# Kernel tuning notes

Hardware: AMD Instinct MI355X
Metric: run time of the kernel (lower is better)

Reference implementation:

```python
import jax, jax.numpy as jnp
import numpy as np

OVERLAP_THRESH = 0.5
NEG_POS_RATIO = 3
VARIANCE = (0.1, 0.2)


def point_form(boxes):
    # center-size (cx,cy,w,h) -> corner (xmin,ymin,xmax,ymax)
    return jnp.concatenate([boxes[:, :2] - boxes[:, 2:] / 2,
                            boxes[:, :2] + boxes[:, 2:] / 2], axis=1)


def jaccard(a, b):
    # a: [O,4] corner boxes, b: [P,4] corner boxes -> IoU [O,P]
    lt = jnp.maximum(a[:, None, :2], b[None, :, :2])
    rb = jnp.minimum(a[:, None, 2:], b[None, :, 2:])
    wh = jnp.clip(rb - lt, 0.0)
    inter = wh[..., 0] * wh[..., 1]
    area_a = (a[:, 2] - a[:, 0]) * (a[:, 3] - a[:, 1])
    area_b = (b[:, 2] - b[:, 0]) * (b[:, 3] - b[:, 1])
    return inter / (area_a[:, None] + area_b[None, :] - inter)


def match_one(truths, priors):
    # truths: [O,4] corner form; priors: [P,4] center-size form
    O = truths.shape[0]
    overlaps = jaccard(truths, point_form(priors))          # [O,P]
    best_prior_idx = jnp.argmax(overlaps, axis=1)           # [O]
    best_truth_overlap = jnp.max(overlaps, axis=0)          # [P]
    best_truth_idx = jnp.argmax(overlaps, axis=0)           # [P]
    # force-assign each gt its best prior
    best_truth_overlap = best_truth_overlap.at[best_prior_idx].set(2.0)
    best_truth_idx = best_truth_idx.at[best_prior_idx].set(jnp.arange(O))
    matches = truths[best_truth_idx]                        # [P,4]
    # ARM: labels are all zeros -> conf = 0 + 1 = 1 for matched, 0 otherwise
    conf = jnp.where(best_truth_overlap < OVERLAP_THRESH, 0, 1).astype(jnp.int32)
    # encode(matched, priors, variances)
    g_cxcy = ((matches[:, :2] + matches[:, 2:]) / 2 - priors[:, :2]) / (VARIANCE[0] * priors[:, 2:])
    g_wh = jnp.log((matches[:, 2:] - matches[:, :2]) / priors[:, 2:]) / VARIANCE[1]
    loc = jnp.concatenate([g_cxcy, g_wh], axis=1)           # [P,4]
    return loc, conf


def arm_loss(loc_data, conf_data, priors, targets):
    B, P, _ = loc_data.shape
    truths = targets[:, :, :4]                              # [B,O,4]
    loc_t, conf_t = jax.vmap(lambda t: match_one(t, priors))(truths)
    loc_t = jax.lax.stop_gradient(loc_t)                    # match targets are detached
    conf_t = jax.lax.stop_gradient(conf_t)
    pos = conf_t > 0                                        # [B,P]

    # localization loss: smooth L1 over positive priors, sum reduction
    diff = loc_data - loc_t
    ad = jnp.abs(diff)
    sl1 = jnp.where(ad < 1.0, 0.5 * diff * diff, ad - 0.5)
    loss_l = jnp.sum(sl1 * pos[..., None].astype(loc_data.dtype))

    # per-prior CE for mining and final loss
    lse = jax.nn.logsumexp(conf_data, axis=-1)              # [B,P]
    c_gt = jnp.take_along_axis(conf_data, conf_t[..., None], axis=-1)[..., 0]
    ce = lse - c_gt                                         # [B,P]

    # hard negative mining: rank negatives by CE (positives zeroed out)
    rank_src = jax.lax.stop_gradient(jnp.where(pos, 0.0, ce))
    loss_idx = jnp.argsort(-rank_src, axis=1)
    idx_rank = jnp.argsort(loss_idx, axis=1)
    num_pos = jnp.sum(pos.astype(jnp.int32), axis=1, keepdims=True)  # [B,1]
    num_neg = jnp.minimum(NEG_POS_RATIO * num_pos, P - 1)
    neg = idx_rank < num_neg                                # [B,P]

    mask = (pos | neg).astype(conf_data.dtype)
    loss_c = jnp.sum(ce * mask)

    N = jnp.sum(num_pos).astype(loc_data.dtype)
    return loss_l / N, loss_c / N


def setup_inputs() -> dict:
    key = jax.random.key(0)
    k1, k2, k3, k4, k5, k6 = jax.random.split(key, 6)
    B, P, O = 64, 32768, 16
    loc_data = jax.random.normal(k1, (B, P, 4), dtype=jnp.float32)
    conf_data = jax.random.normal(k2, (B, P, 2), dtype=jnp.float32)
    # priors: center-size form, interior centers, positive w/h
    cxcy = jax.random.uniform(k3, (P, 2), minval=0.05, maxval=0.95)
    wh = jax.random.uniform(k4, (P, 2), minval=0.02, maxval=0.30)
    priors = jnp.concatenate([cxcy, wh], axis=1).astype(jnp.float32)
    # targets: valid corner-form gt boxes with positive area + label column
    c = jax.random.uniform(k5, (B, O, 2), minval=0.1, maxval=0.9)
    s = jax.random.uniform(k6, (B, O, 2), minval=0.05, maxval=0.4)
    mn = jnp.clip(c - s / 2, 0.0, 1.0)
    mx = jnp.clip(c + s / 2, 0.0, 1.0)
    labels = jnp.ones((B, O, 1), dtype=jnp.float32)
    targets = jnp.concatenate([mn, mx, labels], axis=2).astype(jnp.float32)
    return {"loc_data": loc_data, "conf_data": conf_data, "priors": priors, "targets": targets}


def reference(loc_data, conf_data, priors, targets):
    return arm_loss(loc_data, conf_data, priors, targets)
```

## Files before the change

### kernel.cpp

```cpp
#include <hip/hip_runtime.h>
#include <stdint.h>

#define B_ 64
#define P_ 32768
#define O_ 16
#define BP_CHUNK 1024
#define MCHUNK 4
#define MATCH_BLOCKS (P_ / (512 * MCHUNK) * B_)

constexpr float OVERLAP_THRESH = 0.5f;
constexpr int   NEG_POS_RATIO  = 3;
constexpr float VAR0 = 0.1f;
constexpr float VAR1 = 0.2f;

__device__ __forceinline__ unsigned long long umax64(unsigned long long a,
                                                     unsigned long long b) {
    return a > b ? a : b;
}

__global__ __launch_bounds__(256)
void best_prior_kernel(const float* __restrict__ priors,
                       const float* __restrict__ targets,
                       unsigned long long* __restrict__ bp_pack) {
    int b   = blockIdx.y;
    int tid = threadIdx.x;
    int g   = tid >> 4;
    int o   = tid & 15;

    const float* t = targets + ((size_t)b * O_ + o) * 5;
    float tx0 = t[0], ty0 = t[1], tx1 = t[2], ty1 = t[3];
    float ta  = (tx1 - tx0) * (ty1 - ty0);

    int pbase = blockIdx.x * BP_CHUNK + g;
    float bin_ = 0.f, bun_ = 1.f;
    int   bp_  = pbase;

    #pragma unroll 4
    for (int j = 0; j < BP_CHUNK / 16; ++j) {
        int p = pbase + j * 16;
        float4 pr = ((const float4*)priors)[p];
        float px0 = pr.x - pr.z * 0.5f, py0 = pr.y - pr.w * 0.5f;
        float px1 = pr.x + pr.z * 0.5f, py1 = pr.y + pr.w * 0.5f;
        float pa  = (px1 - px0) * (py1 - py0);
        float w = fmaxf(fminf(tx1, px1) - fmaxf(tx0, px0), 0.f);
        float h = fmaxf(fminf(ty1, py1) - fmaxf(ty0, py0), 0.f);
        float in_ = w * h;
        float un_ = ta + pa - in_;
        bool gt = in_ * bun_ > bin_ * un_;
        bin_ = gt ? in_ : bin_;
        bun_ = gt ? un_ : bun_;
        bp_  = gt ? p   : bp_;
    }

    float iou = bin_ / bun_;
    unsigned long long pack =
        ((unsigned long long)__float_as_uint(iou) << 32) | (unsigned)(~bp_);

    pack = umax64(pack, __shfl_xor(pack, 16, 64));
    pack = umax64(pack, __shfl_xor(pack, 32, 64));

    __shared__ unsigned long long sw[4][16];
    int lane = tid & 63, wid = tid >> 6;
    if (lane < 16) sw[wid][lane] = pack;
    __syncthreads();
    if (tid < 16) {
        unsigned long long m = umax64(umax64(sw[0][tid], sw[1][tid]),
                                      umax64(sw[2][tid], sw[3][tid]));
        atomicMax(&bp_pack[(size_t)b * O_ + tid], m);
    }
}

__device__ __forceinline__ float sl1(float d) {
    float ad = fabsf(d);
    return (ad < 1.f) ? 0.5f * d * d : ad - 0.5f;
}

__global__ __launch_bounds__(256)
void match_kernel(const float* __restrict__ loc_data,
                  const float* __restrict__ conf_data,
                  const float* __restrict__ priors,
                  const float* __restrict__ targets,
                  const unsigned* __restrict__ bp_lo,
                  float* __restrict__ rank,
                  int* __restrict__ num_pos,
                  float2* __restrict__ blk_part) {
    int b    = blockIdx.y;
    int tid  = threadIdx.x;

    __shared__ float4 s_box[O_];
    __shared__ float2 s_meta[O_];
    if (tid < O_) {
        const float* t = targets + ((size_t)b * O_ + tid) * 5;
        float x0 = t[0], y0 = t[1], x1 = t[2], y1 = t[3];
        s_box[tid]  = make_float4(x0, y0, x1, y1);
        int bp = (int)~bp_lo[((size_t)b * O_ + tid) * 2];
        s_meta[tid] = make_float2((x1 - x0) * (y1 - y0), __int_as_float(bp));
    }
    __syncthreads();

    float ll = 0.f, ces = 0.f;
    int   pc = 0;

    for (int c = 0; c < MCHUNK; ++c) {
        int pair = blockIdx.x * (256 * MCHUNK) + c * 256 + tid;
        int p0   = pair * 2;

        float4 prA = ((const float4*)priors)[p0];
        float4 prB = ((const float4*)priors)[p0 + 1];
        float4 cd  = ((const float4*)conf_data)[(size_t)b * (P_ / 2) + pair];

        float ax0 = prA.x - prA.z * 0.5f, ay0 = prA.y - prA.w * 0.5f;
        float ax1 = prA.x + prA.z * 0.5f, ay1 = prA.y + prA.w * 0.5f;
        float bx0 = prB.x - prB.z * 0.5f, by0 = prB.y - prB.w * 0.5f;
        float bx1 = prB.x + prB.z * 0.5f, by1 = prB.y + prB.w * 0.5f;
        float aA = (ax1 - ax0) * (ay1 - ay0);
        float aB = (bx1 - bx0) * (by1 - by0);

        float ibA = 0.f, ubA = 1.f, ibB = 0.f, ubB = 1.f;
        int miA = 0, miB = 0, fiA = -1, fiB = -1;

        #pragma unroll
        for (int o = 0; o < O_; ++o) {
            float4 tb4 = s_box[o];
            float2 mt  = s_meta[o];
            float tx0 = tb4.x, ty0 = tb4.y, tx1 = tb4.z, ty1 = tb4.w;
            float ta  = mt.x;
            int   bp  = __float_as_int(mt.y);

            float wA  = fmaxf(fminf(tx1, ax1) - fmaxf(tx0, ax0), 0.f);
            float hA  = fmaxf(fminf(ty1, ay1) - fmaxf(ty0, ay0), 0.f);
            float inA = wA * hA;
            float unA = ta + aA - inA;
            bool  gA  = inA * ubA > ibA * unA;
            ibA = gA ? inA : ibA;  ubA = gA ? unA : ubA;  miA = gA ? o : miA;
            if (bp == p0) fiA = o;

            float wB  = fmaxf(fminf(tx1, bx1) - fmaxf(tx0, bx0), 0.f);
            float hB  = fmaxf(fminf(ty1, by1) - fmaxf(ty0, by0), 0.f);
            float inB = wB * hB;
            float unB = ta + aB - inB;
            bool  gB  = inB * ubB > ibB * unB;
            ibB = gB ? inB : ibB;  ubB = gB ? unB : ubB;  miB = gB ? o : miB;
            if (bp == p0 + 1) fiB = o;
        }

        bool posA = (fiA >= 0) || (2.f * ibA >= ubA);
        bool posB = (fiB >= 0) || (2.f * ibB >= ubB);

        float mA  = fmaxf(cd.x, cd.y);
        float ceA = mA + __logf(1.f + __expf(-fabsf(cd.x - cd.y))) - (posA ? cd.y : cd.x);
        float mB  = fmaxf(cd.z, cd.w);
        float ceB = mB + __logf(1.f + __expf(-fabsf(cd.z - cd.w))) - (posB ? cd.w : cd.z);

        float2 rk;
        rk.x = posA ? 0.f : ceA;
        rk.y = posB ? 0.f : ceB;
        *(float2*)(rank + (size_t)b * P_ + p0) = rk;

        if (posA) {
            int mi = (fiA >= 0) ? fiA : miA;
            float4 tb4 = s_box[mi];
            float pz = ax1 - ax0, pw = ay1 - ay0;
            float cx = (ax0 + ax1) * 0.5f, cy = (ay0 + ay1) * 0.5f;
            float gcx = __fdividef((tb4.x + tb4.z) * 0.5f - cx, VAR0 * pz);
            float gcy = __fdividef((tb4.y + tb4.w) * 0.5f - cy, VAR0 * pw);
            float gw  = __logf(__fdividef(tb4.z - tb4.x, pz)) * (1.f / VAR1);
            float gh  = __logf(__fdividef(tb4.w - tb4.y, pw)) * (1.f / VAR1);
            float4 ld = ((const float4*)loc_data)[(size_t)b * P_ + p0];
            ll  += sl1(ld.x - gcx) + sl1(ld.y - gcy) + sl1(ld.z - gw) + sl1(ld.w - gh);
            ces += ceA;
            pc  += 1;
        }
        if (posB) {
            int mi = (fiB >= 0) ? fiB : miB;
            float4 tb4 = s_box[mi];
            float pz = bx1 - bx0, pw = by1 - by0;
            float cx = (bx0 + bx1) * 0.5f, cy = (by0 + by1) * 0.5f;
            float gcx = __fdividef((tb4.x + tb4.z) * 0.5f - cx, VAR0 * pz);
            float gcy = __fdividef((tb4.y + tb4.w) * 0.5f - cy, VAR0 * pw);
            float gw  = __logf(__fdividef(tb4.z - tb4.x, pz)) * (1.f / VAR1);
            float gh  = __logf(__fdividef(tb4.w - tb4.y, pw)) * (1.f / VAR1);
            float4 ld = ((const float4*)loc_data)[(size_t)b * P_ + p0 + 1];
            ll  += sl1(ld.x - gcx) + sl1(ld.y - gcy) + sl1(ld.z - gw) + sl1(ld.w - gh);
            ces += ceB;
            pc  += 1;
        }
    }

    for (int off = 32; off; off >>= 1) {
        ll  += __shfl_down(ll, off, 64);
        ces += __shfl_down(ces, off, 64);
        pc  += __shfl_down(pc, off, 64);
    }
    __shared__ float sll[4], sce[4];
    __shared__ int   spc[4];
    int wid = tid >> 6;
    if ((tid & 63) == 0) { sll[wid] = ll; sce[wid] = ces; spc[wid] = pc; }
    __syncthreads();
    if (tid == 0) {
        int tp = spc[0] + spc[1] + spc[2] + spc[3];
        float tl = sll[0] + sll[1] + sll[2] + sll[3];
        float tc = sce[0] + sce[1] + sce[2] + sce[3];
        blk_part[blockIdx.y * gridDim.x + blockIdx.x] = make_float2(tl, tc);
        if (tp) atomicAdd(&num_pos[b], tp);
    }
}

__global__ __launch_bounds__(1024)
void topk_kernel(const float* __restrict__ rank,
                 const int* __restrict__ num_pos,
                 const float2* __restrict__ blk_part,
                 unsigned long long* __restrict__ blk_topk,
                 unsigned* __restrict__ counter,
                 float* __restrict__ out) {
    int b   = blockIdx.x;
    int tid = threadIdx.x;
    int np  = num_pos[b];
    int k   = min(NEG_POS_RATIO * np, P_ - 1);

    __shared__ unsigned cnt[2048];
    __shared__ unsigned wsum[16];
    __shared__ unsigned s_pre;
    __shared__ int      s_k;
    __shared__ unsigned s_ticket;
    int lane = tid & 63, wid = tid >> 6;

    double total = 0.0;
    if (k > 0) {
        const uint4* r4 = (const uint4*)(rank + (size_t)b * P_);
        unsigned key[32];
        #pragma unroll
        for (int j = 0; j < 8; ++j) {
            uint4 v = r4[j * 1024 + tid];
            key[j * 4 + 0] = v.x; key[j * 4 + 1] = v.y;
            key[j * 4 + 2] = v.z; key[j * 4 + 3] = v.w;
        }

        unsigned pre = 0;
        int kk = k;
        #pragma unroll
        for (int level = 0; level < 3; ++level) {
            const int shift = (level == 0) ? 21 : (level == 1) ? 10 : 0;
            const int hishf = (level == 1) ? 21 : 10;
            const unsigned fmask = (level == 2) ? 0x3FFu : 0x7FFu;
            const int nb = (level == 2) ? 1024 : 2048;

            cnt[tid] = 0; cnt[tid + 1024] = 0;
            __syncthreads();

            if (level == 0) {
                #pragma unroll
                for (int j = 0; j < 32; ++j)
                    atomicAdd(&cnt[key[j] >> 21], 1u);
            } else {
                #pragma unroll
                for (int j = 0; j < 32; ++j) {
                    unsigned u = key[j];
                    if ((u >> hishf) == pre) atomicAdd(&cnt[(u >> shift) & fmask], 1u);
                }
            }
            __syncthreads();

            unsigned c1 = (2 * tid + 1 < nb) ? cnt[2 * tid + 1] : 0u;
            unsigned c0 = ((2 * tid < nb) ? cnt[2 * tid] : 0u) + c1;
            unsigned g = c0, G = g;
            #pragma unroll
            for (int off = 1; off < 64; off <<= 1) {
                unsigned r = __shfl_down(G, off, 64);
                if (lane + off < 64) G += r;
            }
            if (lane == 0) wsum[wid] = G;
            __syncthreads();
            unsigned T = 0;
            for (int w = wid + 1; w < 16; ++w) T += wsum[w];
            unsigned A  = (G - g) + T;
            unsigned S1 = A + c1;
            unsigned S0 = A + c0;
            unsigned ukk = (unsigned)kk;
            if (2 * tid + 1 < nb && S1 >= ukk && A < ukk) {
                s_pre = (unsigned)(2 * tid + 1); s_k = kk - (int)A;
            } else if (2 * tid < nb && S0 >= ukk && S1 < ukk) {
                s_pre = (unsigned)(2 * tid);     s_k = kk - (int)S1;
            }
            __syncthreads();
            pre = (pre << ((level == 2) ? 10 : 11)) | s_pre;
            kk  = s_k;
            __syncthreads();
        }

        unsigned kth = pre;
        double sum = 0.0;
        int cg = 0;
        #pragma unroll
        for (int j = 0; j < 32; ++j) {
            unsigned u = key[j];
            if (u > kth) { sum += (double)__uint_as_float(u); ++cg; }
        }
        for (int off = 32; off; off >>= 1) {
            sum += __shfl_down(sum, off, 64);
            cg  += __shfl_down(cg, off, 64);
        }
        __shared__ double ssum[16];
        __shared__ int    scg[16];
        if (lane == 0) { ssum[wid] = sum; scg[wid] = cg; }
        __syncthreads();
        if (tid == 0) {
            double tsum = 0.0; int tcg = 0;
            for (int i = 0; i < 16; ++i) { tsum += ssum[i]; tcg += scg[i]; }
            total = tsum + (double)(k - tcg) * (double)__uint_as_float(kth);
        }
    }

    if (tid == 0) {
        atomicExch(&blk_topk[b], (unsigned long long)__double_as_longlong(total));
        __threadfence();
        s_ticket = atomicAdd(counter, 1u);
    }
    __syncthreads();
    if (s_ticket != B_ - 1) return;

    __threadfence();
    double ll = 0.0, ce = 0.0;
    if (tid < MATCH_BLOCKS) {
        float2 v = blk_part[tid];
        ll = (double)v.x;
        ce = (double)v.y;
    }
    int n = (tid < B_) ? num_pos[tid] : 0;
    double tk = (tid < B_)
        ? __longlong_as_double((long long)atomicAdd(&blk_topk[tid], 0ull))
        : 0.0;

    for (int off = 32; off; off >>= 1) {
        ll += __shfl_down(ll, off, 64);
        ce += __shfl_down(ce, off, 64);
        tk += __shfl_down(tk, off, 64);
        n  += __shfl_down(n, off, 64);
    }
    __shared__ double fll[16], fce[16], ftk[16];
    __shared__ int    fn[16];
    if (lane == 0) { fll[wid] = ll; fce[wid] = ce; ftk[wid] = tk; fn[wid] = n; }
    __syncthreads();
    if (tid == 0) {
        double tll = 0.0, tce = 0.0, ttk = 0.0; int tn = 0;
        for (int i = 0; i < 16; ++i) {
            tll += fll[i]; tce += fce[i]; ttk += ftk[i]; tn += fn[i];
        }
        double Nd = (double)tn;
        out[0] = (float)(tll / Nd);
        out[1] = (float)((tce + ttk) / Nd);
    }
}

extern "C" void kernel_launch(void* const* d_in, const int* in_sizes, int n_in,
                              void* d_out, int out_size, void* d_ws, size_t ws_size,
                              hipStream_t stream) {
    const float* loc_data  = (const float*)d_in[0];
    const float* conf_data = (const float*)d_in[1];
    const float* priors    = (const float*)d_in[2];
    const float* targets   = (const float*)d_in[3];

    char* ws = (char*)d_ws;
    unsigned long long* bp_pack  = (unsigned long long*)ws;
    int*                num_pos  = (int*)(ws + 8192);
    unsigned*           counter  = (unsigned*)(ws + 8448);
    unsigned long long* blk_topk = (unsigned long long*)(ws + 8704);
    float2*             blk_part = (float2*)(ws + 16384);
    float*              rank     = (float*)(ws + 65536);

    hipMemsetAsync(ws, 0, 8512, stream);

    best_prior_kernel<<<dim3(P_ / BP_CHUNK, B_), 256, 0, stream>>>(
        priors, targets, bp_pack);
    match_kernel<<<dim3(P_ / (512 * MCHUNK), B_), 256, 0, stream>>>(
        loc_data, conf_data, priors, targets, (const unsigned*)bp_pack,
        rank, num_pos, blk_part);
    topk_kernel<<<B_, 1024, 0, stream>>>(rank, num_pos, blk_part, blk_topk,
                                         counter, (float*)d_out);
}
```

Measured before the change: 81.68 us.

## Fuse top-k hard-negative selection into match kernel via last-block-per-batch ticket

The separate 1024-thread topk kernel is removed. Its radix-select work now runs in the last match block to finish for each batch, chosen with a per-batch atomic ticket, and a global ticket triggers the final reduction. The aim is to drop one kernel launch and let top-k for early batches overlap with matching for later ones. In exchange, the top-k runs on only 256 threads and re-reads the rank array from global memory (likely from L2) on every radix pass instead of keeping it in registers.

Measured after the change: 190.8 us. 134% more time.

```diff
diff --git a/kernel.cpp b/kernel.cpp
--- a/kernel.cpp
+++ b/kernel.cpp
@@ -6,7 +6,8 @@
 #define O_ 16
 #define BP_CHUNK 1024
 #define MCHUNK 4
-#define MATCH_BLOCKS (P_ / (512 * MCHUNK) * B_)
+#define NBLK_PER_B (P_ / (512 * MCHUNK))
+#define MATCH_BLOCKS (NBLK_PER_B * B_)
 
 constexpr float OVERLAP_THRESH = 0.5f;
 constexpr int   NEG_POS_RATIO  = 3;
@@ -76,16 +77,20 @@
 }
 
 __global__ __launch_bounds__(256)
-void match_kernel(const float* __restrict__ loc_data,
-                  const float* __restrict__ conf_data,
-                  const float* __restrict__ priors,
-                  const float* __restrict__ targets,
-                  const unsigned* __restrict__ bp_lo,
-                  float* __restrict__ rank,
-                  int* __restrict__ num_pos,
-                  float2* __restrict__ blk_part) {
-    int b    = blockIdx.y;
-    int tid  = threadIdx.x;
+void match_topk_kernel(const float* __restrict__ loc_data,
+                       const float* __restrict__ conf_data,
+                       const float* __restrict__ priors,
+                       const float* __restrict__ targets,
+                       const unsigned* __restrict__ bp_lo,
+                       float* __restrict__ rank,
+                       int* __restrict__ num_pos,
+                       float2* __restrict__ blk_part,
+                       unsigned long long* __restrict__ blk_topk,
+                       unsigned* __restrict__ bcnt,
+                       unsigned* __restrict__ gcnt,
+                       float* __restrict__ out) {
+    int b   = blockIdx.y;
+    int tid = threadIdx.x;
 
     __shared__ float4 s_box[O_];
     __shared__ float2 s_meta[O_];
@@ -194,50 +199,37 @@
     }
     __shared__ float sll[4], sce[4];
     __shared__ int   spc[4];
-    int wid = tid >> 6;
-    if ((tid & 63) == 0) { sll[wid] = ll; sce[wid] = ces; spc[wid] = pc; }
-    __syncthreads();
+    int lane = tid & 63, wid = tid >> 6;
+    if (lane == 0) { sll[wid] = ll; sce[wid] = ces; spc[wid] = pc; }
+    __syncthreads();
+    __shared__ unsigned s_t;
     if (tid == 0) {
         int tp = spc[0] + spc[1] + spc[2] + spc[3];
         float tl = sll[0] + sll[1] + sll[2] + sll[3];
         float tc = sce[0] + sce[1] + sce[2] + sce[3];
-        blk_part[blockIdx.y * gridDim.x + blockIdx.x] = make_float2(tl, tc);
+        blk_part[b * NBLK_PER_B + blockIdx.x] = make_float2(tl, tc);
         if (tp) atomicAdd(&num_pos[b], tp);
-    }
-}
-
-__global__ __launch_bounds__(1024)
-void topk_kernel(const float* __restrict__ rank,
-                 const int* __restrict__ num_pos,
-                 const float2* __restrict__ blk_part,
-                 unsigned long long* __restrict__ blk_topk,
-                 unsigned* __restrict__ counter,
-                 float* __restrict__ out) {
-    int b   = blockIdx.x;
-    int tid = threadIdx.x;
-    int np  = num_pos[b];
-    int k   = min(NEG_POS_RATIO * np, P_ - 1);
+        __threadfence();
+        s_t = atomicAdd(&bcnt[b], 1u);
+    }
+    __syncthreads();
+    if (s_t != NBLK_PER_B - 1) return;
+
+    __threadfence();
+    int np = num_pos[b];
+    int k  = min(NEG_POS_RATIO * np, P_ - 1);
 
     __shared__ unsigned cnt[2048];
-    __shared__ unsigned wsum[16];
+    __shared__ unsigned wsum[4];
     __shared__ unsigned s_pre;
     __shared__ int      s_k;
-    __shared__ unsigned s_ticket;
-    int lane = tid & 63, wid = tid >> 6;
 
     double total = 0.0;
     if (k > 0) {
         const uint4* r4 = (const uint4*)(rank + (size_t)b * P_);
-        unsigned key[32];
-        #pragma unroll
-        for (int j = 0; j < 8; ++j) {
-            uint4 v = r4[j * 1024 + tid];
-            key[j * 4 + 0] = v.x; key[j * 4 + 1] = v.y;
-            key[j * 4 + 2] = v.z; key[j * 4 + 3] = v.w;
-        }
-
         unsigned pre = 0;
         int kk = k;
+
         #pragma unroll
         for (int level = 0; level < 3; ++level) {
             const int shift = (level == 0) ? 21 : (level == 1) ? 10 : 0;
@@ -245,25 +237,36 @@
             const unsigned fmask = (level == 2) ? 0x3FFu : 0x7FFu;
             const int nb = (level == 2) ? 1024 : 2048;
 
-            cnt[tid] = 0; cnt[tid + 1024] = 0;
-            __syncthreads();
-
-            if (level == 0) {
-                #pragma unroll
-                for (int j = 0; j < 32; ++j)
-                    atomicAdd(&cnt[key[j] >> 21], 1u);
-            } else {
-                #pragma unroll
-                for (int j = 0; j < 32; ++j) {
-                    unsigned u = key[j];
-                    if ((u >> hishf) == pre) atomicAdd(&cnt[(u >> shift) & fmask], 1u);
+            #pragma unroll
+            for (int i = 0; i < 8; ++i) cnt[i * 256 + tid] = 0;
+            __syncthreads();
+
+            #pragma unroll 4
+            for (int j = 0; j < 32; ++j) {
+                uint4 v = r4[j * 256 + tid];
+                if (level == 0) {
+                    atomicAdd(&cnt[v.x >> 21], 1u);
+                    atomicAdd(&cnt[v.y >> 21], 1u);
+                    atomicAdd(&cnt[v.z >> 21], 1u);
+                    atomicAdd(&cnt[v.w >> 21], 1u);
+                } else {
+                    if ((v.x >> hishf) == pre) atomicAdd(&cnt[(v.x >> shift) & fmask], 1u);
+                    if ((v.y >> hishf) == pre) atomicAdd(&cnt[(v.y >> shift) & fmask], 1u);
+                    if ((v.z >> hishf) == pre) atomicAdd(&cnt[(v.z >> shift) & fmask], 1u);
+                    if ((v.w >> hishf) == pre) atomicAdd(&cnt[(v.w >> shift) & fmask], 1u);
                 }
             }
             __syncthreads();
 
-            unsigned c1 = (2 * tid + 1 < nb) ? cnt[2 * tid + 1] : 0u;
-            unsigned c0 = ((2 * tid < nb) ? cnt[2 * tid] : 0u) + c1;
-            unsigned g = c0, G = g;
+            unsigned suf[9];
+            suf[8] = 0;
+            #pragma unroll
+            for (int j = 7; j >= 0; --j) {
+                int bin = 8 * tid + j;
+                unsigned cj = (bin < nb) ? cnt[bin] : 0u;
+                suf[j] = suf[j + 1] + cj;
+            }
+            unsigned g = suf[0], G = g;
             #pragma unroll
             for (int off = 1; off < 64; off <<= 1) {
                 unsigned r = __shfl_down(G, off, 64);
@@ -272,18 +275,20 @@
             if (lane == 0) wsum[wid] = G;
             __syncthreads();
             unsigned T = 0;
-            for (int w = wid + 1; w < 16; ++w) T += wsum[w];
-            unsigned A  = (G - g) + T;
-            unsigned S1 = A + c1;
-            unsigned S0 = A + c0;
+            for (int w = wid + 1; w < 4; ++w) T += wsum[w];
+            unsigned A = (G - g) + T;
             unsigned ukk = (unsigned)kk;
-            if (2 * tid + 1 < nb && S1 >= ukk && A < ukk) {
-                s_pre = (unsigned)(2 * tid + 1); s_k = kk - (int)A;
-            } else if (2 * tid < nb && S0 >= ukk && S1 < ukk) {
-                s_pre = (unsigned)(2 * tid);     s_k = kk - (int)S1;
+            #pragma unroll
+            for (int j = 0; j < 8; ++j) {
+                unsigned Sj = A + suf[j];
+                unsigned Sn = A + suf[j + 1];
+                if (8 * tid + j < nb && Sj >= ukk && Sn < ukk) {
+                    s_pre = (unsigned)(8 * tid + j);
+                    s_k   = kk - (int)Sn;
+                }
             }
             __syncthreads();
-            pre = (pre << ((level == 2) ? 10 : 11)) | s_pre;
+            pre = (level == 0) ? s_pre : ((pre << ((level == 2) ? 10 : 11)) | s_pre);
             kk  = s_k;
             __syncthreads();
         }
@@ -291,22 +296,25 @@
         unsigned kth = pre;
         double sum = 0.0;
         int cg = 0;
-        #pragma unroll
+        #pragma unroll 4
         for (int j = 0; j < 32; ++j) {
-            unsigned u = key[j];
-            if (u > kth) { sum += (double)__uint_as_float(u); ++cg; }
+            uint4 v = r4[j * 256 + tid];
+            if (v.x > kth) { sum += (double)__uint_as_float(v.x); ++cg; }
+            if (v.y > kth) { sum += (double)__uint_as_float(v.y); ++cg; }
+            if (v.z > kth) { sum += (double)__uint_as_float(v.z); ++cg; }
+            if (v.w > kth) { sum += (double)__uint_as_float(v.w); ++cg; }
         }
         for (int off = 32; off; off >>= 1) {
             sum += __shfl_down(sum, off, 64);
             cg  += __shfl_down(cg, off, 64);
         }
-        __shared__ double ssum[16];
-        __shared__ int    scg[16];
+        __shared__ double ssum[4];
+        __shared__ int    scg[4];
         if (lane == 0) { ssum[wid] = sum; scg[wid] = cg; }
         __syncthreads();
         if (tid == 0) {
-            double tsum = 0.0; int tcg = 0;
-            for (int i = 0; i < 16; ++i) { tsum += ssum[i]; tcg += scg[i]; }
+            double tsum = ssum[0] + ssum[1] + ssum[2] + ssum[3];
+            int    tcg  = scg[0] + scg[1] + scg[2] + scg[3];
             total = tsum + (double)(k - tcg) * (double)__uint_as_float(kth);
         }
     }
@@ -314,17 +322,18 @@
     if (tid == 0) {
         atomicExch(&blk_topk[b], (unsigned long long)__double_as_longlong(total));
         __threadfence();
-        s_ticket = atomicAdd(counter, 1u);
-    }
-    __syncthreads();
-    if (s_ticket != B_ - 1) return;
+        s_t = atomicAdd(gcnt, 1u);
+    }
+    __syncthreads();
+    if (s_t != B_ - 1) return;
 
     __threadfence();
-    double ll = 0.0, ce = 0.0;
-    if (tid < MATCH_BLOCKS) {
-        float2 v = blk_part[tid];
-        ll = (double)v.x;
-        ce = (double)v.y;
+    double fll = 0.0, fce = 0.0;
+    #pragma unroll
+    for (int j = 0; j < MATCH_BLOCKS / 256; ++j) {
+        float2 v = blk_part[j * 256 + tid];
+        fll += (double)v.x;
+        fce += (double)v.y;
     }
     int n = (tid < B_) ? num_pos[tid] : 0;
     double tk = (tid < B_)
@@ -332,20 +341,20 @@
         : 0.0;
 
     for (int off = 32; off; off >>= 1) {
-        ll += __shfl_down(ll, off, 64);
-        ce += __shfl_down(ce, off, 64);
-        tk += __shfl_down(tk, off, 64);
-        n  += __shfl_down(n, off, 64);
-    }
-    __shared__ double fll[16], fce[16], ftk[16];
-    __shared__ int    fn[16];
-    if (lane == 0) { fll[wid] = ll; fce[wid] = ce; ftk[wid] = tk; fn[wid] = n; }
+        fll += __shfl_down(fll, off, 64);
+        fce += __shfl_down(fce, off, 64);
+        tk  += __shfl_down(tk, off, 64);
+        n   += __shfl_down(n, off, 64);
+    }
+    __shared__ double rll[4], rce[4], rtk[4];
+    __shared__ int    rn[4];
+    if (lane == 0) { rll[wid] = fll; rce[wid] = fce; rtk[wid] = tk; rn[wid] = n; }
     __syncthreads();
     if (tid == 0) {
-        double tll = 0.0, tce = 0.0, ttk = 0.0; int tn = 0;
-        for (int i = 0; i < 16; ++i) {
-            tll += fll[i]; tce += fce[i]; ttk += ftk[i]; tn += fn[i];
-        }
+        double tll = rll[0] + rll[1] + rll[2] + rll[3];
+        double tce = rce[0] + rce[1] + rce[2] + rce[3];
+        double ttk = rtk[0] + rtk[1] + rtk[2] + rtk[3];
+        int    tn  = rn[0] + rn[1] + rn[2] + rn[3];
         double Nd = (double)tn;
         out[0] = (float)(tll / Nd);
         out[1] = (float)((tce + ttk) / Nd);
@@ -363,18 +372,17 @@
     char* ws = (char*)d_ws;
     unsigned long long* bp_pack  = (unsigned long long*)ws;
     int*                num_pos  = (int*)(ws + 8192);
-    unsigned*           counter  = (unsigned*)(ws + 8448);
-    unsigned long long* blk_topk = (unsigned long long*)(ws + 8704);
+    unsigned*           bcnt     = (unsigned*)(ws + 8448);
+    unsigned*           gcnt     = (unsigned*)(ws + 8704);
+    unsigned long long* blk_topk = (unsigned long long*)(ws + 8768);
     float2*             blk_part = (float2*)(ws + 16384);
     float*              rank     = (float*)(ws + 65536);
 
-    hipMemsetAsync(ws, 0, 8512, stream);
+    hipMemsetAsync(ws, 0, 8768, stream);
 
     best_prior_kernel<<<dim3(P_ / BP_CHUNK, B_), 256, 0, stream>>>(
         priors, targets, bp_pack);
-    match_kernel<<<dim3(P_ / (512 * MCHUNK), B_), 256, 0, stream>>>(
+    match_topk_kernel<<<dim3(NBLK_PER_B, B_), 256, 0, stream>>>(
         loc_data, conf_data, priors, targets, (const unsigned*)bp_pack,
-        rank, num_pos, blk_part);
-    topk_kernel<<<B_, 1024, 0, stream>>>(rank, num_pos, blk_part, blk_topk,
-                                         counter, (float*)d_out);
-}
+        rank, num_pos, blk_part, blk_topk, bcnt, gcnt, (float*)d_out);
+}
```
